# Optimization experiments

Measured on AMD Instinct MI355X. Metric: run time of the kernel, lower is better.

Reference implementation:

```python
import jax, jax.numpy as jnp
import numpy as np

B, H, T, D = 2, 16, 2048, 64
R1, R2 = 4, 8


def setup_inputs() -> dict:
    key = jax.random.key(0)
    ks = jax.random.split(key, 7)
    return {
        "q": jax.random.normal(ks[0], (B, H, T, D), dtype=jnp.float32),
        "k": jax.random.normal(ks[1], (B, H, T, D), dtype=jnp.float32),
        "v": jax.random.normal(ks[2], (B, H, T, D), dtype=jnp.float32),
        "W_q": jax.random.normal(ks[3], (H, D, R1 * R2), dtype=jnp.float32) / np.sqrt(D),
        "W_k": jax.random.normal(ks[4], (H, D, R1 * R2), dtype=jnp.float32) / np.sqrt(D),
        "core1": jax.random.normal(ks[5], (H, R1), dtype=jnp.float32),
        "core2": jax.random.normal(ks[6], (H, R2), dtype=jnp.float32),
    }


def reference(q, k, v, W_q, W_k, core1, core2):
    """Kronecker low-rank (LSR) causal attention.

    scores[b,h,m,n] = (1/sqrt(R1*R2)) * sum_r kron[h,r] * (q@W_q)[b,h,m,r] * (k@W_k)[b,h,n,r]
    where kron[h] = core1[h] (x) core2[h]  (per-head Kronecker product).
    """
    Hh, r1 = core1.shape
    r2 = core2.shape[1]
    # per-head Kronecker core vector: (H, R1*R2)
    kron = (core1[:, :, None] * core2[:, None, :]).reshape(Hh, r1 * r2)
    scale = 1.0 / jnp.sqrt(jnp.float32(r1 * r2))
    # low-rank projections, rank R = R1*R2
    q_lr = jnp.einsum("bhtd,hdr->bhtr", q, W_q) * kron[None, :, None, :]  # [B,H,T,R]
    k_lr = jnp.einsum("bhtd,hdr->bhtr", k, W_k)                            # [B,H,T,R]
    scores = jnp.einsum("bhmr,bhnr->bhmn", q_lr, k_lr) * scale             # [B,H,T,T]
    t = q.shape[2]
    causal = jnp.tril(jnp.ones((t, t), dtype=bool))
    scores = jnp.where(causal[None, None], scores, -jnp.inf)
    p = jax.nn.softmax(scores, axis=-1)
    return jnp.einsum("bhmn,bhnd->bhmd", p, v)
```

## Files before the change

### kernel.cpp

```cpp
#include <hip/hip_runtime.h>

typedef _Float16 f16;
typedef _Float16 f16x2 __attribute__((ext_vector_type(2)));
typedef _Float16 f16x4 __attribute__((ext_vector_type(4)));
typedef _Float16 f16x8 __attribute__((ext_vector_type(8)));
typedef float    f32x4 __attribute__((ext_vector_type(4)));
typedef float    f32x16 __attribute__((ext_vector_type(16)));

constexpr int B_ = 2, H_ = 16, T_ = 2048, D_ = 64, R_ = 32, NT = 32;
constexpr int NROW = B_ * H_ * T_;

__device__ __forceinline__ f32x4 mfma16(f16x8 a, f16x8 b, f32x4 c) {
  return __builtin_amdgcn_mfma_f32_16x16x32_f16(a, b, c, 0, 0, 0);
}
__device__ __forceinline__ f32x16 mfma32(f16x8 a, f16x8 b, f32x16 c) {
  return __builtin_amdgcn_mfma_f32_32x32x16_f16(a, b, c, 0, 0, 0);
}
__device__ __forceinline__ void ld_lds16(const void* g, void* l) {
  __builtin_amdgcn_global_load_lds(
      (const __attribute__((address_space(1))) unsigned int*)g,
      (__attribute__((address_space(3))) unsigned int*)l, 16, 0, 0);
}

__global__ __launch_bounds__(256) void proj_kernel(
    const float* __restrict__ q, const float* __restrict__ k, const float* __restrict__ v,
    const float* __restrict__ Wq, const float* __restrict__ Wk,
    const float* __restrict__ c1, const float* __restrict__ c2,
    f16* __restrict__ qlr, f16* __restrict__ klr, f16* __restrict__ vt)
{
  __shared__ float sv[64 * 65];

  const int tid = threadIdx.x, w = tid >> 6, lane = tid & 63;
  const int l15 = lane & 15, l4 = lane >> 4;
  const int bh = blockIdx.x >> 5, h = bh & (H_ - 1);
  const int t0 = (blockIdx.x & 31) * 64;

  const float* vb = v + ((size_t)bh * T_ + t0) * D_;
  float4 vld[4];
#pragma unroll
  for (int it = 0; it < 4; ++it) vld[it] = ((const float4*)vb)[it * 256 + tid];

  const int m = t0 + 16 * w + l15;
  const float* qr = q + ((size_t)bh * T_ + m) * D_;
  const float* kr = k + ((size_t)bh * T_ + m) * D_;
  f16x8 aq[2], ak[2];
#pragma unroll
  for (int kc = 0; kc < 2; ++kc) {
    float4 x0 = *(const float4*)(qr + kc * 32 + 8 * l4);
    float4 x1 = *(const float4*)(qr + kc * 32 + 8 * l4 + 4);
    float4 y0 = *(const float4*)(kr + kc * 32 + 8 * l4);
    float4 y1 = *(const float4*)(kr + kc * 32 + 8 * l4 + 4);
    f16x8 A, K;
    A[0]=(f16)x0.x; A[1]=(f16)x0.y; A[2]=(f16)x0.z; A[3]=(f16)x0.w;
    A[4]=(f16)x1.x; A[5]=(f16)x1.y; A[6]=(f16)x1.z; A[7]=(f16)x1.w;
    K[0]=(f16)y0.x; K[1]=(f16)y0.y; K[2]=(f16)y0.z; K[3]=(f16)y0.w;
    K[4]=(f16)y1.x; K[5]=(f16)y1.y; K[6]=(f16)y1.z; K[7]=(f16)y1.w;
    aq[kc] = A; ak[kc] = K;
  }

  const float* Wqh = Wq + (size_t)h * D_ * R_;
  const float* Wkh = Wk + (size_t)h * D_ * R_;
  f16x8 bq[2][2], bk[2][2];
#pragma unroll
  for (int kc = 0; kc < 2; ++kc)
#pragma unroll
    for (int nt = 0; nt < 2; ++nt) {
      const int r = 16 * nt + l15;
      f16x8 q8, k8;
#pragma unroll
      for (int j2 = 0; j2 < 8; ++j2) {
        const int d = kc * 32 + 8 * l4 + j2;
        q8[j2] = (f16)Wqh[d * R_ + r];
        k8[j2] = (f16)Wkh[d * R_ + r];
      }
      bq[kc][nt] = q8; bk[kc][nt] = k8;
    }

#pragma unroll
  for (int it = 0; it < 4; ++it) {
    const int i4 = it * 256 + tid, t = i4 >> 4, dq = (i4 & 15) * 4;
    sv[t * 65 + dq    ] = vld[it].x;
    sv[t * 65 + dq + 1] = vld[it].y;
    sv[t * 65 + dq + 2] = vld[it].z;
    sv[t * 65 + dq + 3] = vld[it].w;
  }

  const f32x4 z4 = {0.f, 0.f, 0.f, 0.f};
#pragma unroll
  for (int nt = 0; nt < 2; ++nt) {
    f32x4 accq = mfma16(aq[0], bq[0][nt], z4);
    accq = mfma16(aq[1], bq[1][nt], accq);
    f32x4 acck = mfma16(ak[0], bk[0][nt], z4);
    acck = mfma16(ak[1], bk[1][nt], acck);
    const int r = 16 * nt + l15;
    const float scl = c1[h * 4 + (r >> 3)] * c2[h * 8 + (r & 7)] *
                      (0.17677669529663687f * 1.4426950408889634f);
#pragma unroll
    for (int i = 0; i < 4; ++i) {
      const size_t row = (size_t)bh * T_ + t0 + 16 * w + 4 * l4 + i;
      qlr[row * R_ + r] = (f16)(accq[i] * scl);
      klr[row * R_ + r] = (f16)acck[i];
    }
  }

  __syncthreads();
#pragma unroll
  for (int it = 0; it < 8; ++it) {
    const int idx = it * 256 + tid, d = idx >> 5, t = (idx & 31) * 2;
    const float f0 = sv[t * 65 + d], f1 = sv[t * 65 + 65 + d];
    f16x2 pr; pr[0] = (f16)f0; pr[1] = (f16)f1;
    const int sw = ((((t >> 3) ^ (d & 7)) << 3) | (t & 7));
    *(f16x2*)(vt + ((size_t)bh * D_ + d) * T_ + t0 + sw) = pr;
  }
}

__global__ __launch_bounds__(128) void attn_kernel(
    const f16* __restrict__ qlr, const f16* __restrict__ klr,
    const f16* __restrict__ vt, f16* __restrict__ On, float2* __restrict__ ml,
    const int NS)
{
  __shared__ __align__(16) f16 s_k[64 * 32];
  __shared__ __align__(16) f16 s_vt[64 * 64];
  __shared__ __align__(16) f16 s_p[2][32 * 64];

  const int tid = threadIdx.x, w = tid >> 6, lane = tid & 63;
  const int l15 = lane & 15, l4 = lane >> 4, l31 = lane & 31, hh = lane >> 5;
  const int bh = blockIdx.x & 31;
  const int rest = blockIdx.x >> 5;
  const int nsl = (NS == 4) ? 2 : (NS == 2) ? 1 : 0;
  const int mt = 31 - (rest >> nsl);
  const int s  = rest & (NS - 1);
  const int m0 = mt * 64;

  const f16x8 aq0 = *(const f16x8*)(qlr + ((size_t)bh * T_ + m0 + 32 * w + l15) * R_ + 8 * l4);
  const f16x8 aq1 = *(const f16x8*)(qlr + ((size_t)bh * T_ + m0 + 32 * w + 16 + l15) * R_ + 8 * l4);

  const f16* kb = klr + (size_t)bh * T_ * R_;
  const f16* vb = vt + (size_t)bh * D_ * T_;

  f32x16 oacc[2];
#pragma unroll
  for (int c = 0; c < 2; ++c)
#pragma unroll
    for (int e = 0; e < 16; ++e) oacc[c][e] = 0.f;
  float mi0 = -1e30f, mi1 = -1e30f, li0 = 0.f, li1 = 0.f;
  const f32x4 z4 = {0.f, 0.f, 0.f, 0.f};

  for (int j = s; j <= mt; j += NS) {
    const int n0 = 64 * j;
    __syncthreads();
#pragma unroll
    for (int e = 0; e < 2; ++e)
      ld_lds16((const char*)kb + (size_t)n0 * 64 + (2 * w + e) * 1024 + lane * 16,
               (char*)s_k + (2 * w + e) * 1024);
#pragma unroll
    for (int e = 0; e < 4; ++e) {
      const int d0 = w * 32 + e * 8;
      ld_lds16((const char*)vb + ((size_t)(d0 + (lane >> 3)) * T_ + n0) * 2 + (lane & 7) * 16,
               (char*)s_vt + d0 * 128);
    }
    __syncthreads();

    f32x4 sc[4][2];
#pragma unroll
    for (int ns = 0; ns < 4; ++ns) {
      f16x8 akf = *(const f16x8*)&s_k[(16 * ns + l15) * 32 + 8 * l4];
      sc[ns][0] = mfma16(akf, aq0, z4);
      sc[ns][1] = mfma16(akf, aq1, z4);
    }
    if (j == mt) {
      const int lim0 = 32 * w + l15;
#pragma unroll
      for (int ns = 0; ns < 4; ++ns) {
        const int nb = 16 * ns + 4 * l4;
#pragma unroll
        for (int i = 0; i < 4; ++i) {
          if (nb + i > lim0)      sc[ns][0][i] = -1e30f;
          if (nb + i > lim0 + 16) sc[ns][1][i] = -1e30f;
        }
      }
    }

    float rm0 = -1e30f, rm1 = -1e30f;
#pragma unroll
    for (int ns = 0; ns < 4; ++ns)
#pragma unroll
      for (int i = 0; i < 4; ++i) {
        rm0 = fmaxf(rm0, sc[ns][0][i]);
        rm1 = fmaxf(rm1, sc[ns][1][i]);
      }
    rm0 = fmaxf(rm0, __shfl_xor(rm0, 16)); rm0 = fmaxf(rm0, __shfl_xor(rm0, 32));
    rm1 = fmaxf(rm1, __shfl_xor(rm1, 16)); rm1 = fmaxf(rm1, __shfl_xor(rm1, 32));
    const float mn0 = fmaxf(mi0, rm0), mn1 = fmaxf(mi1, rm1);
    const float a0 = exp2f(mi0 - mn0), a1 = exp2f(mi1 - mn1);
    float rs0 = 0.f, rs1 = 0.f;
#pragma unroll
    for (int ns = 0; ns < 4; ++ns) {
      f16x4 p0v, p1v;
#pragma unroll
      for (int i = 0; i < 4; ++i) {
        const float p0 = exp2f(sc[ns][0][i] - mn0);
        const float p1 = exp2f(sc[ns][1][i] - mn1);
        rs0 += p0; rs1 += p1;
        p0v[i] = (f16)p0; p1v[i] = (f16)p1;
      }
      const int col = ((((2 * ns + (l4 >> 1)) ^ (l15 & 7)) << 3) | (4 * (l4 & 1)));
      *(f16x4*)&s_p[w][l15 * 64 + col]        = p0v;
      *(f16x4*)&s_p[w][(16 + l15) * 64 + col] = p1v;
    }
    rs0 += __shfl_xor(rs0, 16); rs0 += __shfl_xor(rs0, 32);
    rs1 += __shfl_xor(rs1, 16); rs1 += __shfl_xor(rs1, 32);
    li0 = li0 * a0 + rs0; li1 = li1 * a1 + rs1;
    mi0 = mn0; mi1 = mn1;
    const float aPV = (lane & 16) ? a1 : a0;
#pragma unroll
    for (int c = 0; c < 2; ++c) oacc[c] *= aPV;

#pragma unroll
    for (int kc = 0; kc < 4; ++kc) {
      const int u = (2 * kc + hh) ^ (l31 & 7);
      f16x8 bp = *(const f16x8*)&s_p[w][l31 * 64 + u * 8];
#pragma unroll
      for (int c = 0; c < 2; ++c) {
        f16x8 av = *(const f16x8*)&s_vt[(32 * c + l31) * 64 + u * 8];
        oacc[c] = mfma32(av, bp, oacc[c]);
      }
    }
  }

  const float myl = (lane & 16) ? li1 : li0;
  const float invl = myl > 0.f ? 1.f / myl : 0.f;
  f16* ob = On + (((size_t)s * 32 + bh) * T_ + m0 + 32 * w + l31) * D_;
#pragma unroll
  for (int c = 0; c < 2; ++c)
#pragma unroll
    for (int g = 0; g < 4; ++g) {
      f16x4 o;
#pragma unroll
      for (int e = 0; e < 4; ++e) o[e] = (f16)(oacc[c][4 * g + e] * invl);
      *(f16x4*)(ob + 32 * c + 8 * g + 4 * hh) = o;
    }
  if (l4 < 2) {
    float2 mlv;
    mlv.x = l4 ? mi1 : mi0;
    mlv.y = l4 ? li1 : li0;
    ml[((size_t)s * 32 + bh) * T_ + m0 + 32 * w + 16 * l4 + l15] = mlv;
  }
}

__global__ __launch_bounds__(256) void merge_kernel(
    const f16* __restrict__ On, const float2* __restrict__ ml,
    float* __restrict__ out, const int NS)
{
  const int row = blockIdx.x * 32 + (threadIdx.x >> 3);
  const int d0 = (threadIdx.x & 7) * 8;
  float res[8];
  if (NS == 4) {
    const float2 a0 = ml[row];
    const float2 a1 = ml[1 * NROW + row];
    const float2 a2 = ml[2 * NROW + row];
    const float2 a3 = ml[3 * NROW + row];
    const f16x8 o0 = *(const f16x8*)(On + (size_t)row * 64 + d0);
    const f16x8 o1 = *(const f16x8*)(On + ((size_t)1 * NROW + row) * 64 + d0);
    const f16x8 o2 = *(const f16x8*)(On + ((size_t)2 * NROW + row) * 64 + d0);
    const f16x8 o3 = *(const f16x8*)(On + ((size_t)3 * NROW + row) * 64 + d0);
    const float ms = fmaxf(fmaxf(a0.x, a1.x), fmaxf(a2.x, a3.x));
    const float w0 = exp2f(a0.x - ms) * a0.y;
    const float w1 = exp2f(a1.x - ms) * a1.y;
    const float w2 = exp2f(a2.x - ms) * a2.y;
    const float w3 = exp2f(a3.x - ms) * a3.y;
    const float inv = 1.f / (w0 + w1 + w2 + w3);
    const float c0 = w0 * inv, c1 = w1 * inv, c2 = w2 * inv, c3 = w3 * inv;
#pragma unroll
    for (int e = 0; e < 8; ++e)
      res[e] = c0 * (float)o0[e] + c1 * (float)o1[e] + c2 * (float)o2[e] + c3 * (float)o3[e];
  } else if (NS == 2) {
    const float2 a = ml[row];
    const float2 b = ml[NROW + row];
    const f16x8 o0 = *(const f16x8*)(On + (size_t)row * 64 + d0);
    const f16x8 o1 = *(const f16x8*)(On + ((size_t)NROW + row) * 64 + d0);
    const float ms = fmaxf(a.x, b.x);
    const float w0 = exp2f(a.x - ms) * a.y;
    const float w1 = exp2f(b.x - ms) * b.y;
    const float inv = 1.f / (w0 + w1);
    const float c0 = w0 * inv, c1 = w1 * inv;
#pragma unroll
    for (int e = 0; e < 8; ++e) res[e] = c0 * (float)o0[e] + c1 * (float)o1[e];
  } else {
    const f16x8 o0 = *(const f16x8*)(On + (size_t)row * 64 + d0);
#pragma unroll
    for (int e = 0; e < 8; ++e) res[e] = (float)o0[e];
  }
  float* ob = out + (size_t)row * 64 + d0;
  f32x4 r0, r1;
#pragma unroll
  for (int e = 0; e < 4; ++e) { r0[e] = res[e]; r1[e] = res[4 + e]; }
  *(f32x4*)ob = r0;
  *(f32x4*)(ob + 4) = r1;
}

extern "C" void kernel_launch(void* const* d_in, const int* in_sizes, int n_in,
                              void* d_out, int out_size, void* d_ws, size_t ws_size,
                              hipStream_t stream) {
  const float* q  = (const float*)d_in[0];
  const float* k  = (const float*)d_in[1];
  const float* v  = (const float*)d_in[2];
  const float* Wq = (const float*)d_in[3];
  const float* Wk = (const float*)d_in[4];
  const float* c1 = (const float*)d_in[5];
  const float* c2 = (const float*)d_in[6];
  float* out = (float*)d_out;

  const size_t MB = 1 << 20;
  int NS = 1;
  if (ws_size >= 16 * MB + 4 * (8 * MB + NROW * sizeof(float2))) NS = 4;
  else if (ws_size >= 16 * MB + 2 * (8 * MB + NROW * sizeof(float2))) NS = 2;

  f16* qlr = (f16*)d_ws;
  f16* klr = qlr + (size_t)B_ * H_ * T_ * R_;
  f16* vt  = klr + (size_t)B_ * H_ * T_ * R_;
  f16* On  = vt + (size_t)B_ * H_ * T_ * D_;
  float2* ml = (float2*)(On + (size_t)NS * NROW * D_);

  proj_kernel<<<B_ * H_ * NT, 256, 0, stream>>>(q, k, v, Wq, Wk, c1, c2, qlr, klr, vt);
  attn_kernel<<<B_ * H_ * NT * NS, 128, 0, stream>>>(qlr, klr, vt, On, ml, NS);
  merge_kernel<<<NROW / 32, 256, 0, stream>>>(On, ml, out, NS);
}
```

Baseline: 158.8 us.

## Split attention tile across four waves with 16x16 MFMA for PV

The attention block grows from 2 to 4 waves, so each wave owns 16 query rows instead of 32. The PV product now uses 16x16x32 MFMAs instead of 32x32x16, and the K/V tile loads are spread over four waves. This should raise per-block parallelism and cut per-wave register pressure, which may help latency hiding. The cost is more waves sharing each loaded K/V tile, plus smaller MFMA shapes with more LDS reads per flop.

```diff
diff --git a/kernel.cpp b/kernel.cpp
--- a/kernel.cpp
+++ b/kernel.cpp
@@ -12,9 +12,6 @@
 
 __device__ __forceinline__ f32x4 mfma16(f16x8 a, f16x8 b, f32x4 c) {
   return __builtin_amdgcn_mfma_f32_16x16x32_f16(a, b, c, 0, 0, 0);
-}
-__device__ __forceinline__ f32x16 mfma32(f16x8 a, f16x8 b, f32x16 c) {
-  return __builtin_amdgcn_mfma_f32_32x32x16_f16(a, b, c, 0, 0, 0);
 }
 __device__ __forceinline__ void ld_lds16(const void* g, void* l) {
   __builtin_amdgcn_global_load_lds(
@@ -114,17 +111,17 @@
   }
 }
 
-__global__ __launch_bounds__(128) void attn_kernel(
+__global__ __launch_bounds__(256) void attn_kernel(
     const f16* __restrict__ qlr, const f16* __restrict__ klr,
     const f16* __restrict__ vt, f16* __restrict__ On, float2* __restrict__ ml,
     const int NS)
 {
   __shared__ __align__(16) f16 s_k[64 * 32];
   __shared__ __align__(16) f16 s_vt[64 * 64];
-  __shared__ __align__(16) f16 s_p[2][32 * 64];
+  __shared__ __align__(16) f16 s_p[4][16 * 64];
 
   const int tid = threadIdx.x, w = tid >> 6, lane = tid & 63;
-  const int l15 = lane & 15, l4 = lane >> 4, l31 = lane & 31, hh = lane >> 5;
+  const int l15 = lane & 15, l4 = lane >> 4;
   const int bh = blockIdx.x & 31;
   const int rest = blockIdx.x >> 5;
   const int nsl = (NS == 4) ? 2 : (NS == 2) ? 1 : 0;
@@ -132,119 +129,98 @@
   const int s  = rest & (NS - 1);
   const int m0 = mt * 64;
 
-  const f16x8 aq0 = *(const f16x8*)(qlr + ((size_t)bh * T_ + m0 + 32 * w + l15) * R_ + 8 * l4);
-  const f16x8 aq1 = *(const f16x8*)(qlr + ((size_t)bh * T_ + m0 + 32 * w + 16 + l15) * R_ + 8 * l4);
+  const f16x8 aq = *(const f16x8*)(qlr + ((size_t)bh * T_ + m0 + 16 * w + l15) * R_ + 8 * l4);
 
   const f16* kb = klr + (size_t)bh * T_ * R_;
   const f16* vb = vt + (size_t)bh * D_ * T_;
 
-  f32x16 oacc[2];
-#pragma unroll
-  for (int c = 0; c < 2; ++c)
-#pragma unroll
-    for (int e = 0; e < 16; ++e) oacc[c][e] = 0.f;
-  float mi0 = -1e30f, mi1 = -1e30f, li0 = 0.f, li1 = 0.f;
   const f32x4 z4 = {0.f, 0.f, 0.f, 0.f};
+  f32x4 oacc[4];
+#pragma unroll
+  for (int d = 0; d < 4; ++d) oacc[d] = z4;
+  float mi = -1e30f, li = 0.f;
 
   for (int j = s; j <= mt; j += NS) {
     const int n0 = 64 * j;
     __syncthreads();
-#pragma unroll
-    for (int e = 0; e < 2; ++e)
-      ld_lds16((const char*)kb + (size_t)n0 * 64 + (2 * w + e) * 1024 + lane * 16,
-               (char*)s_k + (2 * w + e) * 1024);
-#pragma unroll
-    for (int e = 0; e < 4; ++e) {
-      const int d0 = w * 32 + e * 8;
+    ld_lds16((const char*)kb + (size_t)n0 * 64 + w * 1024 + lane * 16,
+             (char*)s_k + w * 1024);
+#pragma unroll
+    for (int e = 0; e < 2; ++e) {
+      const int d0 = 16 * w + e * 8;
       ld_lds16((const char*)vb + ((size_t)(d0 + (lane >> 3)) * T_ + n0) * 2 + (lane & 7) * 16,
                (char*)s_vt + d0 * 128);
     }
     __syncthreads();
 
-    f32x4 sc[4][2];
+    f32x4 sc[4];
 #pragma unroll
     for (int ns = 0; ns < 4; ++ns) {
       f16x8 akf = *(const f16x8*)&s_k[(16 * ns + l15) * 32 + 8 * l4];
-      sc[ns][0] = mfma16(akf, aq0, z4);
-      sc[ns][1] = mfma16(akf, aq1, z4);
+      sc[ns] = mfma16(akf, aq, z4);
     }
     if (j == mt) {
-      const int lim0 = 32 * w + l15;
+      const int lim = 16 * w + l15;
 #pragma unroll
       for (int ns = 0; ns < 4; ++ns) {
         const int nb = 16 * ns + 4 * l4;
 #pragma unroll
-        for (int i = 0; i < 4; ++i) {
-          if (nb + i > lim0)      sc[ns][0][i] = -1e30f;
-          if (nb + i > lim0 + 16) sc[ns][1][i] = -1e30f;
-        }
+        for (int i = 0; i < 4; ++i)
+          if (nb + i > lim) sc[ns][i] = -1e30f;
       }
     }
 
-    float rm0 = -1e30f, rm1 = -1e30f;
+    float rm = -1e30f;
 #pragma unroll
     for (int ns = 0; ns < 4; ++ns)
 #pragma unroll
+      for (int i = 0; i < 4; ++i) rm = fmaxf(rm, sc[ns][i]);
+    rm = fmaxf(rm, __shfl_xor(rm, 16));
+    rm = fmaxf(rm, __shfl_xor(rm, 32));
+    const float mn = fmaxf(mi, rm);
+    const float a = exp2f(mi - mn);
+    float rs = 0.f;
+#pragma unroll
+    for (int ns = 0; ns < 4; ++ns) {
+      f16x4 pf;
+#pragma unroll
       for (int i = 0; i < 4; ++i) {
-        rm0 = fmaxf(rm0, sc[ns][0][i]);
-        rm1 = fmaxf(rm1, sc[ns][1][i]);
-      }
-    rm0 = fmaxf(rm0, __shfl_xor(rm0, 16)); rm0 = fmaxf(rm0, __shfl_xor(rm0, 32));
-    rm1 = fmaxf(rm1, __shfl_xor(rm1, 16)); rm1 = fmaxf(rm1, __shfl_xor(rm1, 32));
-    const float mn0 = fmaxf(mi0, rm0), mn1 = fmaxf(mi1, rm1);
-    const float a0 = exp2f(mi0 - mn0), a1 = exp2f(mi1 - mn1);
-    float rs0 = 0.f, rs1 = 0.f;
-#pragma unroll
-    for (int ns = 0; ns < 4; ++ns) {
-      f16x4 p0v, p1v;
-#pragma unroll
-      for (int i = 0; i < 4; ++i) {
-        const float p0 = exp2f(sc[ns][0][i] - mn0);
-        const float p1 = exp2f(sc[ns][1][i] - mn1);
-        rs0 += p0; rs1 += p1;
-        p0v[i] = (f16)p0; p1v[i] = (f16)p1;
+        const float p = exp2f(sc[ns][i] - mn);
+        rs += p; pf[i] = (f16)p;
       }
       const int col = ((((2 * ns + (l4 >> 1)) ^ (l15 & 7)) << 3) | (4 * (l4 & 1)));
-      *(f16x4*)&s_p[w][l15 * 64 + col]        = p0v;
-      *(f16x4*)&s_p[w][(16 + l15) * 64 + col] = p1v;
-    }
-    rs0 += __shfl_xor(rs0, 16); rs0 += __shfl_xor(rs0, 32);
-    rs1 += __shfl_xor(rs1, 16); rs1 += __shfl_xor(rs1, 32);
-    li0 = li0 * a0 + rs0; li1 = li1 * a1 + rs1;
-    mi0 = mn0; mi1 = mn1;
-    const float aPV = (lane & 16) ? a1 : a0;
-#pragma unroll
-    for (int c = 0; c < 2; ++c) oacc[c] *= aPV;
-
-#pragma unroll
-    for (int kc = 0; kc < 4; ++kc) {
-      const int u = (2 * kc + hh) ^ (l31 & 7);
-      f16x8 bp = *(const f16x8*)&s_p[w][l31 * 64 + u * 8];
-#pragma unroll
-      for (int c = 0; c < 2; ++c) {
-        f16x8 av = *(const f16x8*)&s_vt[(32 * c + l31) * 64 + u * 8];
-        oacc[c] = mfma32(av, bp, oacc[c]);
+      *(f16x4*)&s_p[w][l15 * 64 + col] = pf;
+    }
+    rs += __shfl_xor(rs, 16);
+    rs += __shfl_xor(rs, 32);
+    li = li * a + rs; mi = mn;
+#pragma unroll
+    for (int d = 0; d < 4; ++d) oacc[d] *= a;
+
+#pragma unroll
+    for (int nk = 0; nk < 2; ++nk) {
+      const int u = (4 * nk + l4) ^ (l15 & 7);
+      f16x8 bp = *(const f16x8*)&s_p[w][l15 * 64 + u * 8];
+#pragma unroll
+      for (int dblk = 0; dblk < 4; ++dblk) {
+        f16x8 av = *(const f16x8*)&s_vt[(16 * dblk + l15) * 64 + u * 8];
+        oacc[dblk] = mfma16(av, bp, oacc[dblk]);
       }
     }
   }
 
-  const float myl = (lane & 16) ? li1 : li0;
-  const float invl = myl > 0.f ? 1.f / myl : 0.f;
-  f16* ob = On + (((size_t)s * 32 + bh) * T_ + m0 + 32 * w + l31) * D_;
-#pragma unroll
-  for (int c = 0; c < 2; ++c)
-#pragma unroll
-    for (int g = 0; g < 4; ++g) {
-      f16x4 o;
-#pragma unroll
-      for (int e = 0; e < 4; ++e) o[e] = (f16)(oacc[c][4 * g + e] * invl);
-      *(f16x4*)(ob + 32 * c + 8 * g + 4 * hh) = o;
-    }
-  if (l4 < 2) {
-    float2 mlv;
-    mlv.x = l4 ? mi1 : mi0;
-    mlv.y = l4 ? li1 : li0;
-    ml[((size_t)s * 32 + bh) * T_ + m0 + 32 * w + 16 * l4 + l15] = mlv;
+  const float invl = li > 0.f ? 1.f / li : 0.f;
+  f16* ob = On + (((size_t)s * 32 + bh) * T_ + m0 + 16 * w + l15) * D_;
+#pragma unroll
+  for (int dblk = 0; dblk < 4; ++dblk) {
+    f16x4 o;
+#pragma unroll
+    for (int i = 0; i < 4; ++i) o[i] = (f16)(oacc[dblk][i] * invl);
+    *(f16x4*)(ob + 16 * dblk + 4 * l4) = o;
+  }
+  if (l4 == 0) {
+    float2 mlv; mlv.x = mi; mlv.y = li;
+    ml[((size_t)s * 32 + bh) * T_ + m0 + 16 * w + l15] = mlv;
   }
 }
 
@@ -323,6 +299,6 @@
   float2* ml = (float2*)(On + (size_t)NS * NROW * D_);
 
   proj_kernel<<<B_ * H_ * NT, 256, 0, stream>>>(q, k, v, Wq, Wk, c1, c2, qlr, klr, vt);
-  attn_kernel<<<B_ * H_ * NT * NS, 128, 0, stream>>>(qlr, klr, vt, On, ml, NS);
+  attn_kernel<<<B_ * H_ * NT * NS, 256, 0, stream>>>(qlr, klr, vt, On, ml, NS);
   merge_kernel<<<NROW / 32, 256, 0, stream>>>(On, ml, out, NS);
 }
```

After: 148.5 us. 6.5% less time.
